# Kernel tuning notes

Measured on AMD Instinct MI355X. Metric: run time of the kernel, lower is better.

## Reference

```python
import jax, jax.numpy as jnp
import numpy as np

H = 16  # num_heads


def _rotate_half(t):
    d = t.shape[-1] // 2
    return jnp.concatenate((-t[..., d:], t[..., :d]), axis=-1)


def setup_inputs() -> dict:
    key = jax.random.key(0)
    ks = jax.random.split(key, 4)
    S, HID = 2048, 1280
    D = HID // H  # 80
    x = jax.random.normal(ks[0], (S, HID), dtype=jnp.float32)
    # rotary tables (seq_len, head_dim)
    inv_freq = 1.0 / (10000.0 ** (jnp.arange(0, D, 2, dtype=jnp.float32) / D))
    freqs = jnp.arange(S, dtype=jnp.float32)[:, None] * inv_freq[None, :]  # (S, D/2)
    emb = jnp.concatenate([freqs, freqs], axis=-1)  # (S, D)
    cos = jnp.cos(emb)
    sin = jnp.sin(emb)
    W_qkv = jax.random.normal(ks[1], (HID, 3 * HID), dtype=jnp.float32) * 0.02
    b_qkv = jnp.zeros((3 * HID,), dtype=jnp.float32)
    W_out = jax.random.normal(ks[2], (HID, HID), dtype=jnp.float32) * 0.02
    b_out = jnp.zeros((HID,), dtype=jnp.float32)
    # 8 windows of 256 tokens each -> block-diagonal attention
    cu_seqlens = jnp.arange(0, S + 1, 256, dtype=jnp.int32)  # (9,)
    return {"x": x, "cos": cos, "sin": sin, "W_qkv": W_qkv, "b_qkv": b_qkv,
            "W_out": W_out, "b_out": b_out, "cu_seqlens": cu_seqlens}


def _segment_mask(cu_seqlens, seq_len, dtype):
    positions = jnp.arange(seq_len)
    starts = cu_seqlens[:-1]
    ends = cu_seqlens[1:]
    in_segment = (positions[:, None] >= starts[None, :]) & (positions[:, None] < ends[None, :])
    segment_ids = jnp.argmax(in_segment.astype(jnp.int32), axis=-1)  # (S,)
    same_segment = segment_ids[:, None] == segment_ids[None, :]      # (S, S)
    return jnp.where(same_segment, jnp.zeros((), dtype), jnp.finfo(dtype).min)


def reference(x, cos, sin, W_qkv, b_qkv, W_out, b_out, cu_seqlens):
    S, HID = x.shape
    D = HID // H
    scale = D ** -0.5
    qkv = x @ W_qkv + b_qkv                       # (S, 3*HID)
    q, k, v = jnp.split(qkv, 3, axis=-1)
    q = q.reshape(S, H, D)
    k = k.reshape(S, H, D)
    v = v.reshape(S, H, D)
    cos_f = cos[:, :D][:, None, :]                # (S, 1, D)
    sin_f = sin[:, :D][:, None, :]
    q = q * cos_f + _rotate_half(q) * sin_f       # inline RoPE (fp32)
    k = k * cos_f + _rotate_half(k) * sin_f
    q = jnp.transpose(q, (1, 0, 2))               # (H, S, D)
    k = jnp.transpose(k, (1, 0, 2))
    v = jnp.transpose(v, (1, 0, 2))
    scores = jnp.einsum('hqd,hkd->hqk', q, k) * scale  # (H, S, S)
    mask = _segment_mask(cu_seqlens, S, scores.dtype)  # (S, S) block-diagonal bias
    scores = scores + mask[None, :, :]
    weights = jax.nn.softmax(scores, axis=-1)
    out = jnp.einsum('hqk,hkd->hqd', weights, v)       # (H, S, D)
    out = jnp.transpose(out, (1, 0, 2)).reshape(S, HID)
    return out @ W_out + b_out
```

## Files before the change

### kernel.cpp

```cpp
#include <hip/hip_runtime.h>


typedef short s16x8 __attribute__((ext_vector_type(8)));
typedef __bf16 bf16x8 __attribute__((ext_vector_type(8)));
typedef float f32x4 __attribute__((ext_vector_type(4)));
typedef unsigned short u16;
typedef unsigned long long u64;

__device__ __forceinline__ f32x4 mfma16(s16x8 a, s16x8 b, f32x4 c) {
  return __builtin_amdgcn_mfma_f32_16x16x32_bf16(
      __builtin_bit_cast(bf16x8, a), __builtin_bit_cast(bf16x8, b), c, 0, 0, 0);
}
__device__ __forceinline__ u16 f2b(float f) {
  union { float f; unsigned u; } v;
  v.f = f;
  unsigned r = v.u + 0x7fffu + ((v.u >> 16) & 1u);
  return (u16)(r >> 16);
}
__device__ __forceinline__ void gl16(const u16* g, u16* l) {
  __builtin_amdgcn_global_load_lds(
      (const __attribute__((address_space(1))) unsigned int*)(const void*)g,
      (__attribute__((address_space(3))) unsigned int*)(void*)l, 16, 0, 0);
}

__device__ __forceinline__ void transpose_body(const float* __restrict__ W,
                                               u16* __restrict__ WT, int K, int N,
                                               int nb, int kb, int t, float (*tile)[33]) {
  int tx = t & 31, ty = t >> 5;
#pragma unroll
  for (int r = 0; r < 32; r += 8)
    tile[ty + r][tx] = W[(long)(kb + ty + r) * N + nb + tx];
  __syncthreads();
#pragma unroll
  for (int r = 0; r < 32; r += 8)
    WT[(long)(nb + ty + r) * K + kb + tx] = f2b(tile[tx][ty + r]);
}

__global__ __launch_bounds__(256) void prep(const float* __restrict__ x,
                                            u16* __restrict__ xb,
                                            const float* __restrict__ Wqkv,
                                            u16* __restrict__ WqkvT,
                                            const float* __restrict__ Wout,
                                            u16* __restrict__ WoutT) {
  __shared__ float tile[32][33];
  int bid = blockIdx.x, t = threadIdx.x;
  if (bid < 2560) {
    int i = bid * 256 + t;
    float4 v = ((const float4*)x)[i];
    u64 pk = (u64)f2b(v.x) | ((u64)f2b(v.y) << 16) | ((u64)f2b(v.z) << 32) |
             ((u64)f2b(v.w) << 48);
    ((u64*)xb)[i] = pk;
  } else if (bid < 7360) {
    int i = bid - 2560;
    transpose_body(Wqkv, WqkvT, 1280, 3840, (i % 120) * 32, (i / 120) * 32, t, tile);
  } else {
    int i = bid - 7360;
    transpose_body(Wout, WoutT, 1280, 1280, (i % 40) * 32, (i / 40) * 32, t, tile);
  }
}

__global__ __launch_bounds__(512, 4) void gemm_qkv_rope(const u16* __restrict__ A,
                                                        const u16* __restrict__ B,
                                                        const float* __restrict__ bias,
                                                        const float* __restrict__ cosb,
                                                        const float* __restrict__ sinb,
                                                        u16* __restrict__ Qr,
                                                        u16* __restrict__ Kr,
                                                        u16* __restrict__ VT) {
  __shared__ u16 As[2][128 * 64];
  __shared__ u16 Bs[2][160 * 64];
  const int K = 1280;
  int i = blockIdx.x;
  int xcd = i & 7, j = i >> 3;
  int n0 = (xcd * 3 + (j % 3)) * 160;
  int m0 = (j / 3) * 128;
  int t = threadIdx.x, w = t >> 6, lane = t & 63, lm = lane & 15, quad = lane >> 4;
  int wm = (w >> 1) * 32, wn = (w & 1) * 80;

  const u16* AgSrc[2];
  const u16* BgSrc[3];
#pragma unroll
  for (int c = 0; c < 2; c++) {
    int g = c * 512 + t, row = g >> 3, chp = g & 7;
    AgSrc[c] = A + (long)(m0 + row) * K + ((chp ^ (row & 7)) << 3);
  }
#pragma unroll
  for (int c = 0; c < 2; c++) {
    int g = c * 512 + t, row = g >> 3, chp = g & 7;
    BgSrc[c] = B + (long)(n0 + row) * K + ((chp ^ (row & 7)) << 3);
  }
  {
    int g = 1024 + t, row = g >> 3, chp = g & 7;
    BgSrc[2] = B + (long)(n0 + row) * K + ((chp ^ (row & 7)) << 3);
  }

  auto stage = [&](int buf, int k0) {
#pragma unroll
    for (int c = 0; c < 2; c++) gl16(AgSrc[c] + k0, &As[buf][c * 4096 + w * 512]);
#pragma unroll
    for (int c = 0; c < 2; c++) gl16(BgSrc[c] + k0, &Bs[buf][c * 4096 + w * 512]);
    if (t < 256) gl16(BgSrc[2] + k0, &Bs[buf][8192 + w * 512]);
  };

  f32x4 acc[2][5] = {};
  stage(0, 0);
  int buf = 0;
  for (int k0 = 0; k0 < K; k0 += 64) {
    __syncthreads();
    if (k0 + 64 < K) stage(buf ^ 1, k0 + 64);
#pragma unroll
    for (int kh = 0; kh < 2; kh++) {
      s16x8 af[2], bfr[5];
#pragma unroll
      for (int mt = 0; mt < 2; mt++) {
        int rm = wm + mt * 16 + lm;
        af[mt] = *(const s16x8*)&As[buf][rm * 64 + (((kh * 4 + quad) ^ (rm & 7)) << 3)];
      }
#pragma unroll
      for (int nt = 0; nt < 5; nt++) {
        int rn = wn + nt * 16 + lm;
        bfr[nt] = *(const s16x8*)&Bs[buf][rn * 64 + (((kh * 4 + quad) ^ (rn & 7)) << 3)];
      }
#pragma unroll
      for (int mt = 0; mt < 2; mt++)
#pragma unroll
        for (int nt = 0; nt < 5; nt++)
          acc[mt][nt] = mfma16(af[mt], bfr[nt], acc[mt][nt]);
    }
    buf ^= 1;
  }

  int region = n0 / 1280;
  int hcol = (n0 - region * 1280 + wn) / 80;
  float bv[5];
#pragma unroll
  for (int nt = 0; nt < 5; nt++) bv[nt] = bias[n0 + wn + nt * 16 + lm];

  if (region == 2) {
#pragma unroll
    for (int mt = 0; mt < 2; mt++) {
      int sbase = m0 + wm + mt * 16 + quad * 4;
#pragma unroll
      for (int nt = 0; nt < 5; nt++) {
        int d = nt * 16 + lm;
        u64 pk = 0;
#pragma unroll
        for (int r = 0; r < 4; r++)
          pk |= (u64)f2b(acc[mt][nt][r] + bv[nt]) << (16 * r);
        *(u64*)&VT[((long)hcol * 80 + d) * 2048 + sbase] = pk;
      }
    }
    return;
  }

  const float scale = 0.111803398874989f;
  bool lo = lm < 8;
  u16* Out = (region == 0) ? Qr : Kr;
  float oscale = (region == 0) ? scale : 1.0f;
#pragma unroll
  for (int mt = 0; mt < 2; mt++)
#pragma unroll
    for (int r = 0; r < 4; r++) {
      int s = m0 + wm + mt * 16 + quad * 4 + r;
      float val[5], sw[5];
#pragma unroll
      for (int nt = 0; nt < 5; nt++) val[nt] = acc[mt][nt][r] + bv[nt];
#pragma unroll
      for (int nt = 0; nt < 5; nt++) sw[nt] = __shfl_xor(val[nt], 8);
      float rot[5];
      rot[0] = -(lo ? sw[2] : sw[3]);
      rot[1] = -(lo ? sw[3] : sw[4]);
      rot[2] = lo ? -sw[4] : sw[0];
      rot[3] = lo ? sw[0] : sw[1];
      rot[4] = lo ? sw[1] : sw[2];
      u16* orow = Out + ((long)hcol * 2048 + s) * 80;
      const float* crow = cosb + s * 80;
      const float* srw = sinb + s * 80;
#pragma unroll
      for (int nt = 0; nt < 5; nt++) {
        int d = nt * 16 + lm;
        orow[d] = f2b((val[nt] * crow[d] + rot[nt] * srw[d]) * oscale);
      }
    }
}

template <bool OUT_F32>
__global__ __launch_bounds__(256) void gemm_bt(const u16* __restrict__ A,
                                               const u16* __restrict__ B,
                                               const float* __restrict__ bias,
                                               void* __restrict__ Cout,
                                               int M, int N, int K) {
  __shared__ u16 As[64 * 32];
  __shared__ u16 Bs[128 * 32];
  int m0 = blockIdx.x * 64, n0 = blockIdx.y * 128;
  int t = threadIdx.x;
  int w = t >> 6, lane = t & 63, lm = lane & 15, quad = lane >> 4;
  int wm = (w >> 1) * 32, wn = (w & 1) * 64;
  int srow = t >> 2;
  int scol = (((t & 3) ^ ((t >> 3) & 3))) * 8;
  const u16* Ag = A + (long)(m0 + srow) * K + scol;
  const u16* Bg = B + (long)(n0 + srow) * K + scol;
  u16* AsW = As + w * 512;
  u16* BsW = Bs + w * 512;
  u16* BsW2 = Bs + 2048 + w * 512;
  f32x4 acc[2][4] = {};
  for (int k0 = 0; k0 < K; k0 += 32) {
    __syncthreads();
    gl16(Ag + k0, AsW);
    gl16(Bg + k0, BsW);
    gl16(Bg + (long)64 * K + k0, BsW2);
    __syncthreads();
    s16x8 af[2], bf[4];
#pragma unroll
    for (int mt = 0; mt < 2; mt++) {
      int rm = wm + mt * 16 + lm;
      af[mt] = *(const s16x8*)&As[rm * 32 + ((quad ^ ((rm >> 1) & 3)) << 3)];
    }
#pragma unroll
    for (int nt = 0; nt < 4; nt++) {
      int rn = wn + nt * 16 + lm;
      bf[nt] = *(const s16x8*)&Bs[rn * 32 + ((quad ^ ((rn >> 1) & 3)) << 3)];
    }
#pragma unroll
    for (int mt = 0; mt < 2; mt++)
#pragma unroll
      for (int nt = 0; nt < 4; nt++)
        acc[mt][nt] = mfma16(af[mt], bf[nt], acc[mt][nt]);
  }
#pragma unroll
  for (int mt = 0; mt < 2; mt++)
#pragma unroll
    for (int nt = 0; nt < 4; nt++) {
      int col = n0 + wn + nt * 16 + lm;
      float bvv = bias[col];
#pragma unroll
      for (int r = 0; r < 4; r++) {
        int row = m0 + wm + mt * 16 + quad * 4 + r;
        float v = acc[mt][nt][r] + bvv;
        if (OUT_F32) ((float*)Cout)[(long)row * N + col] = v;
        else ((u16*)Cout)[(long)row * N + col] = f2b(v);
      }
    }
}

__global__ __launch_bounds__(256, 1) void attn_kernel(const u16* __restrict__ Qr,
                                                      const u16* __restrict__ Kr,
                                                      const u16* __restrict__ VT,
                                                      u16* __restrict__ AO) {
  int qh = blockIdx.x, seg = blockIdx.y, h = blockIdx.z;
  int t = threadIdx.x;
  int w = t >> 6, lane = t & 63, lm = lane & 15, quad = lane >> 4;
  __shared__ u16 Ps[4][32 * 256];

  int s0 = seg * 256 + qh * 128 + w * 32;
  const u16* Qh = Qr + ((long)h * 2048 + s0) * 80;
  const u16* Kh = Kr + ((long)h * 2048 + seg * 256) * 80;

  f32x4 sc[2][16] = {};
  s16x8 zz = {};
#pragma unroll
  for (int kk = 0; kk < 3; kk++) {
    int dbase = kk * 32 + quad * 8;
    bool valid = dbase < 80;
    s16x8 af[2];
#pragma unroll
    for (int mt = 0; mt < 2; mt++)
      af[mt] = valid ? *(const s16x8*)(Qh + (mt * 16 + lm) * 80 + dbase) : zz;
#pragma unroll
    for (int nt = 0; nt < 16; nt++) {
      s16x8 bfr = valid ? *(const s16x8*)(Kh + (nt * 16 + lm) * 80 + dbase) : zz;
#pragma unroll
      for (int mt = 0; mt < 2; mt++)
        sc[mt][nt] = mfma16(af[mt], bfr, sc[mt][nt]);
    }
  }

  float rowinv[8];
#pragma unroll
  for (int mt = 0; mt < 2; mt++)
#pragma unroll
    for (int r = 0; r < 4; r++) {
      float m = sc[mt][0][r];
#pragma unroll
      for (int nt = 1; nt < 16; nt++) m = fmaxf(m, sc[mt][nt][r]);
      m = fmaxf(m, __shfl_xor(m, 1));
      m = fmaxf(m, __shfl_xor(m, 2));
      m = fmaxf(m, __shfl_xor(m, 4));
      m = fmaxf(m, __shfl_xor(m, 8));
      float s = 0.f;
#pragma unroll
      for (int nt = 0; nt < 16; nt++) {
        float e = __expf(sc[mt][nt][r] - m);
        sc[mt][nt][r] = e;
        s += e;
      }
      s += __shfl_xor(s, 1);
      s += __shfl_xor(s, 2);
      s += __shfl_xor(s, 4);
      s += __shfl_xor(s, 8);
      rowinv[mt * 4 + r] = 1.0f / s;
      int row = mt * 16 + quad * 4 + r;
#pragma unroll
      for (int nt = 0; nt < 16; nt++) {
        int chunk = nt * 2 + (lm >> 3);
        Ps[w][row * 256 + ((chunk ^ row) << 3) + (lm & 7)] = f2b(sc[mt][nt][r]);
      }
    }
  asm volatile("s_waitcnt lgkmcnt(0)" ::: "memory");

  f32x4 oacc[2][5] = {};
  const u16* Vh = VT + (long)h * 80 * 2048 + seg * 256;
#pragma unroll
  for (int kc = 0; kc < 8; kc++) {
    s16x8 pa[2];
#pragma unroll
    for (int mt = 0; mt < 2; mt++) {
      int row = mt * 16 + lm;
      pa[mt] = *(const s16x8*)&Ps[w][row * 256 + (((kc * 4 + quad) ^ row) << 3)];
    }
#pragma unroll
    for (int nt = 0; nt < 5; nt++) {
      s16x8 bvv = *(const s16x8*)(Vh + (long)(nt * 16 + lm) * 2048 + kc * 32 + quad * 8);
#pragma unroll
      for (int mt = 0; mt < 2; mt++)
        oacc[mt][nt] = mfma16(pa[mt], bvv, oacc[mt][nt]);
    }
  }
#pragma unroll
  for (int mt = 0; mt < 2; mt++)
#pragma unroll
    for (int nt = 0; nt < 5; nt++)
#pragma unroll
      for (int r = 0; r < 4; r++)
        AO[(long)(s0 + mt * 16 + quad * 4 + r) * 1280 + h * 80 + nt * 16 + lm] =
            f2b(oacc[mt][nt][r] * rowinv[mt * 4 + r]);
}

extern "C" void kernel_launch(void* const* d_in, const int* in_sizes, int n_in,
                              void* d_out, int out_size, void* d_ws, size_t ws_size,
                              hipStream_t stream) {
  const float* x    = (const float*)d_in[0];
  const float* cosb = (const float*)d_in[1];
  const float* sinb = (const float*)d_in[2];
  const float* Wqkv = (const float*)d_in[3];
  const float* bqkv = (const float*)d_in[4];
  const float* Wout = (const float*)d_in[5];
  const float* bout = (const float*)d_in[6];

  char* p = (char*)d_ws;
  u16* xb    = (u16*)p;
  u16* WqkvT = (u16*)(p + 5242880);
  u16* WoutT = (u16*)(p + 15073280);
  u16* Qr    = (u16*)(p + 18350080);
  u16* Kr    = (u16*)(p + 23592960);
  u16* VT    = (u16*)(p + 28835840);
  u16* AO    = xb;

  prep<<<dim3(8960), dim3(256), 0, stream>>>(x, xb, Wqkv, WqkvT, Wout, WoutT);
  gemm_qkv_rope<<<dim3(384), dim3(512), 0, stream>>>(xb, WqkvT, bqkv, cosb, sinb,
                                                     Qr, Kr, VT);
  attn_kernel<<<dim3(2, 8, 16), dim3(256), 0, stream>>>(Qr, Kr, VT, AO);
  gemm_bt<true><<<dim3(32, 10), dim3(256), 0, stream>>>(AO, WoutT, bout, d_out,
                                                        2048, 1280, 1280);
}
```

Baseline: 162.5 us.

## Double-buffer output GEMM with larger K tiles and split attention into smaller row blocks

Replaces the generic output-projection GEMM with a specialised kernel that uses 64x160 tiles, K-steps of 64 and double-buffered LDS loads, so the next tile is fetched while the current one is multiplied and one barrier per step is dropped. Block indices are mapped so each XCD covers a fixed column slice. The attention kernel now gives each wave 16 query rows instead of 32 and launches twice as many blocks, aiming for more parallelism and occupancy. In exchange, each K/V fragment loaded from global memory feeds fewer MFMAs in attention.

```diff
diff --git a/kernel.cpp b/kernel.cpp
--- a/kernel.cpp
+++ b/kernel.cpp
@@ -184,156 +184,150 @@
     }
 }
 
-template <bool OUT_F32>
-__global__ __launch_bounds__(256) void gemm_bt(const u16* __restrict__ A,
-                                               const u16* __restrict__ B,
-                                               const float* __restrict__ bias,
-                                               void* __restrict__ Cout,
-                                               int M, int N, int K) {
-  __shared__ u16 As[64 * 32];
-  __shared__ u16 Bs[128 * 32];
-  int m0 = blockIdx.x * 64, n0 = blockIdx.y * 128;
-  int t = threadIdx.x;
-  int w = t >> 6, lane = t & 63, lm = lane & 15, quad = lane >> 4;
-  int wm = (w >> 1) * 32, wn = (w & 1) * 64;
-  int srow = t >> 2;
-  int scol = (((t & 3) ^ ((t >> 3) & 3))) * 8;
-  const u16* Ag = A + (long)(m0 + srow) * K + scol;
-  const u16* Bg = B + (long)(n0 + srow) * K + scol;
-  u16* AsW = As + w * 512;
-  u16* BsW = Bs + w * 512;
-  u16* BsW2 = Bs + 2048 + w * 512;
-  f32x4 acc[2][4] = {};
-  for (int k0 = 0; k0 < K; k0 += 32) {
+__global__ __launch_bounds__(512, 2) void gemm_out(const u16* __restrict__ A,
+                                                   const u16* __restrict__ B,
+                                                   const float* __restrict__ bias,
+                                                   float* __restrict__ C) {
+  __shared__ u16 As[2][64 * 64];
+  __shared__ u16 Bs[2][160 * 64];
+  const int K = 1280;
+  int i = blockIdx.x;
+  int xcd = i & 7, m0 = (i >> 3) * 64, n0 = xcd * 160;
+  int t = threadIdx.x, w = t >> 6, lane = t & 63, lm = lane & 15, quad = lane >> 4;
+  int wm = (w >> 1) * 16, wn = (w & 1) * 80;
+
+  const u16* AgSrc;
+  {
+    int row = t >> 3, chp = t & 7;
+    AgSrc = A + (long)(m0 + row) * K + ((chp ^ (row & 7)) << 3);
+  }
+  const u16* BgSrc[3];
+#pragma unroll
+  for (int c = 0; c < 2; c++) {
+    int g = c * 512 + t, row = g >> 3, chp = g & 7;
+    BgSrc[c] = B + (long)(n0 + row) * K + ((chp ^ (row & 7)) << 3);
+  }
+  {
+    int g = 1024 + t, row = g >> 3, chp = g & 7;
+    BgSrc[2] = B + (long)(n0 + row) * K + ((chp ^ (row & 7)) << 3);
+  }
+
+  auto stage = [&](int buf, int k0) {
+    gl16(AgSrc + k0, &As[buf][w * 512]);
+#pragma unroll
+    for (int c = 0; c < 2; c++) gl16(BgSrc[c] + k0, &Bs[buf][c * 4096 + w * 512]);
+    if (t < 256) gl16(BgSrc[2] + k0, &Bs[buf][8192 + w * 512]);
+  };
+
+  f32x4 acc[5] = {};
+  stage(0, 0);
+  int buf = 0;
+  for (int k0 = 0; k0 < K; k0 += 64) {
     __syncthreads();
-    gl16(Ag + k0, AsW);
-    gl16(Bg + k0, BsW);
-    gl16(Bg + (long)64 * K + k0, BsW2);
-    __syncthreads();
-    s16x8 af[2], bf[4];
-#pragma unroll
-    for (int mt = 0; mt < 2; mt++) {
-      int rm = wm + mt * 16 + lm;
-      af[mt] = *(const s16x8*)&As[rm * 32 + ((quad ^ ((rm >> 1) & 3)) << 3)];
-    }
-#pragma unroll
-    for (int nt = 0; nt < 4; nt++) {
-      int rn = wn + nt * 16 + lm;
-      bf[nt] = *(const s16x8*)&Bs[rn * 32 + ((quad ^ ((rn >> 1) & 3)) << 3)];
-    }
-#pragma unroll
-    for (int mt = 0; mt < 2; mt++)
-#pragma unroll
-      for (int nt = 0; nt < 4; nt++)
-        acc[mt][nt] = mfma16(af[mt], bf[nt], acc[mt][nt]);
-  }
-#pragma unroll
-  for (int mt = 0; mt < 2; mt++)
-#pragma unroll
-    for (int nt = 0; nt < 4; nt++) {
-      int col = n0 + wn + nt * 16 + lm;
-      float bvv = bias[col];
-#pragma unroll
-      for (int r = 0; r < 4; r++) {
-        int row = m0 + wm + mt * 16 + quad * 4 + r;
-        float v = acc[mt][nt][r] + bvv;
-        if (OUT_F32) ((float*)Cout)[(long)row * N + col] = v;
-        else ((u16*)Cout)[(long)row * N + col] = f2b(v);
-      }
-    }
-}
-
-__global__ __launch_bounds__(256, 1) void attn_kernel(const u16* __restrict__ Qr,
+    if (k0 + 64 < K) stage(buf ^ 1, k0 + 64);
+#pragma unroll
+    for (int kh = 0; kh < 2; kh++) {
+      int rm = wm + lm;
+      s16x8 af = *(const s16x8*)&As[buf][rm * 64 + (((kh * 4 + quad) ^ (rm & 7)) << 3)];
+      s16x8 bfr[5];
+#pragma unroll
+      for (int nt = 0; nt < 5; nt++) {
+        int rn = wn + nt * 16 + lm;
+        bfr[nt] = *(const s16x8*)&Bs[buf][rn * 64 + (((kh * 4 + quad) ^ (rn & 7)) << 3)];
+      }
+#pragma unroll
+      for (int nt = 0; nt < 5; nt++) acc[nt] = mfma16(af, bfr[nt], acc[nt]);
+    }
+    buf ^= 1;
+  }
+#pragma unroll
+  for (int nt = 0; nt < 5; nt++) {
+    int col = n0 + wn + nt * 16 + lm;
+    float bvv = bias[col];
+#pragma unroll
+    for (int r = 0; r < 4; r++) {
+      int row = m0 + wm + quad * 4 + r;
+      C[(long)row * 1280 + col] = acc[nt][r] + bvv;
+    }
+  }
+}
+
+__global__ __launch_bounds__(256, 2) void attn_kernel(const u16* __restrict__ Qr,
                                                       const u16* __restrict__ Kr,
                                                       const u16* __restrict__ VT,
                                                       u16* __restrict__ AO) {
-  int qh = blockIdx.x, seg = blockIdx.y, h = blockIdx.z;
+  int qb = blockIdx.x, seg = blockIdx.y, h = blockIdx.z;
   int t = threadIdx.x;
   int w = t >> 6, lane = t & 63, lm = lane & 15, quad = lane >> 4;
-  __shared__ u16 Ps[4][32 * 256];
-
-  int s0 = seg * 256 + qh * 128 + w * 32;
+  __shared__ u16 Ps[4][16 * 256];
+
+  int s0 = seg * 256 + qb * 64 + w * 16;
   const u16* Qh = Qr + ((long)h * 2048 + s0) * 80;
   const u16* Kh = Kr + ((long)h * 2048 + seg * 256) * 80;
 
-  f32x4 sc[2][16] = {};
+  f32x4 sc[16] = {};
   s16x8 zz = {};
 #pragma unroll
   for (int kk = 0; kk < 3; kk++) {
     int dbase = kk * 32 + quad * 8;
     bool valid = dbase < 80;
-    s16x8 af[2];
-#pragma unroll
-    for (int mt = 0; mt < 2; mt++)
-      af[mt] = valid ? *(const s16x8*)(Qh + (mt * 16 + lm) * 80 + dbase) : zz;
+    s16x8 af = valid ? *(const s16x8*)(Qh + lm * 80 + dbase) : zz;
 #pragma unroll
     for (int nt = 0; nt < 16; nt++) {
       s16x8 bfr = valid ? *(const s16x8*)(Kh + (nt * 16 + lm) * 80 + dbase) : zz;
-#pragma unroll
-      for (int mt = 0; mt < 2; mt++)
-        sc[mt][nt] = mfma16(af[mt], bfr, sc[mt][nt]);
-    }
-  }
-
-  float rowinv[8];
-#pragma unroll
-  for (int mt = 0; mt < 2; mt++)
-#pragma unroll
-    for (int r = 0; r < 4; r++) {
-      float m = sc[mt][0][r];
-#pragma unroll
-      for (int nt = 1; nt < 16; nt++) m = fmaxf(m, sc[mt][nt][r]);
-      m = fmaxf(m, __shfl_xor(m, 1));
-      m = fmaxf(m, __shfl_xor(m, 2));
-      m = fmaxf(m, __shfl_xor(m, 4));
-      m = fmaxf(m, __shfl_xor(m, 8));
-      float s = 0.f;
-#pragma unroll
-      for (int nt = 0; nt < 16; nt++) {
-        float e = __expf(sc[mt][nt][r] - m);
-        sc[mt][nt][r] = e;
-        s += e;
-      }
-      s += __shfl_xor(s, 1);
-      s += __shfl_xor(s, 2);
-      s += __shfl_xor(s, 4);
-      s += __shfl_xor(s, 8);
-      rowinv[mt * 4 + r] = 1.0f / s;
-      int row = mt * 16 + quad * 4 + r;
-#pragma unroll
-      for (int nt = 0; nt < 16; nt++) {
-        int chunk = nt * 2 + (lm >> 3);
-        Ps[w][row * 256 + ((chunk ^ row) << 3) + (lm & 7)] = f2b(sc[mt][nt][r]);
-      }
-    }
+      sc[nt] = mfma16(af, bfr, sc[nt]);
+    }
+  }
+
+  float rowinv[4];
+#pragma unroll
+  for (int r = 0; r < 4; r++) {
+    float m = sc[0][r];
+#pragma unroll
+    for (int nt = 1; nt < 16; nt++) m = fmaxf(m, sc[nt][r]);
+    m = fmaxf(m, __shfl_xor(m, 1));
+    m = fmaxf(m, __shfl_xor(m, 2));
+    m = fmaxf(m, __shfl_xor(m, 4));
+    m = fmaxf(m, __shfl_xor(m, 8));
+    float s = 0.f;
+#pragma unroll
+    for (int nt = 0; nt < 16; nt++) {
+      float e = __expf(sc[nt][r] - m);
+      sc[nt][r] = e;
+      s += e;
+    }
+    s += __shfl_xor(s, 1);
+    s += __shfl_xor(s, 2);
+    s += __shfl_xor(s, 4);
+    s += __shfl_xor(s, 8);
+    rowinv[r] = 1.0f / s;
+    int row = quad * 4 + r;
+#pragma unroll
+    for (int nt = 0; nt < 16; nt++) {
+      int chunk = nt * 2 + (lm >> 3);
+      Ps[w][row * 256 + ((chunk ^ row) << 3) + (lm & 7)] = f2b(sc[nt][r]);
+    }
+  }
   asm volatile("s_waitcnt lgkmcnt(0)" ::: "memory");
 
-  f32x4 oacc[2][5] = {};
+  f32x4 oacc[5] = {};
   const u16* Vh = VT + (long)h * 80 * 2048 + seg * 256;
 #pragma unroll
   for (int kc = 0; kc < 8; kc++) {
-    s16x8 pa[2];
-#pragma unroll
-    for (int mt = 0; mt < 2; mt++) {
-      int row = mt * 16 + lm;
-      pa[mt] = *(const s16x8*)&Ps[w][row * 256 + (((kc * 4 + quad) ^ row) << 3)];
-    }
+    int row = lm;
+    s16x8 pa = *(const s16x8*)&Ps[w][row * 256 + (((kc * 4 + quad) ^ row) << 3)];
 #pragma unroll
     for (int nt = 0; nt < 5; nt++) {
       s16x8 bvv = *(const s16x8*)(Vh + (long)(nt * 16 + lm) * 2048 + kc * 32 + quad * 8);
-#pragma unroll
-      for (int mt = 0; mt < 2; mt++)
-        oacc[mt][nt] = mfma16(pa[mt], bvv, oacc[mt][nt]);
-    }
-  }
-#pragma unroll
-  for (int mt = 0; mt < 2; mt++)
-#pragma unroll
-    for (int nt = 0; nt < 5; nt++)
-#pragma unroll
-      for (int r = 0; r < 4; r++)
-        AO[(long)(s0 + mt * 16 + quad * 4 + r) * 1280 + h * 80 + nt * 16 + lm] =
-            f2b(oacc[mt][nt][r] * rowinv[mt * 4 + r]);
+      oacc[nt] = mfma16(pa, bvv, oacc[nt]);
+    }
+  }
+#pragma unroll
+  for (int nt = 0; nt < 5; nt++)
+#pragma unroll
+    for (int r = 0; r < 4; r++)
+      AO[(long)(s0 + quad * 4 + r) * 1280 + h * 80 + nt * 16 + lm] =
+          f2b(oacc[nt][r] * rowinv[r]);
 }
 
 extern "C" void kernel_launch(void* const* d_in, const int* in_sizes, int n_in,
@@ -359,7 +353,6 @@
   prep<<<dim3(8960), dim3(256), 0, stream>>>(x, xb, Wqkv, WqkvT, Wout, WoutT);
   gemm_qkv_rope<<<dim3(384), dim3(512), 0, stream>>>(xb, WqkvT, bqkv, cosb, sinb,
                                                      Qr, Kr, VT);
-  attn_kernel<<<dim3(2, 8, 16), dim3(256), 0, stream>>>(Qr, Kr, VT, AO);
-  gemm_bt<true><<<dim3(32, 10), dim3(256), 0, stream>>>(AO, WoutT, bout, d_out,
-                                                        2048, 1280, 1280);
-}
+  attn_kernel<<<dim3(4, 8, 16), dim3(256), 0, stream>>>(Qr, Kr, VT, AO);
+  gemm_out<<<dim3(256), dim3(512), 0, stream>>>(AO, WoutT, bout, (float*)d_out);
+}
```

After: 161.8 us. Within noise of the previous version (-0.5%).
